# Kernel optimization log

Hardware: AMD Instinct MI355X
Metric: run time of the kernel (lower is better)

## Reference

```python
import jax, jax.numpy as jnp
import numpy as np

B, H, W_, D, K = 64, 28, 28, 512, 32


def setup_inputs() -> dict:
    key = jax.random.key(0)
    k1, k2, k3 = jax.random.split(key, 3)
    x = jax.random.normal(k1, (B, H, W_, D), dtype=jnp.float32)
    # 1x1 conv weight, no bias: [D_in, K] (he_normal-like scale)
    W = jax.random.normal(k2, (D, K), dtype=jnp.float32) * np.sqrt(2.0 / D)
    # cluster offset tensor C (original shape (1,1,1,512,32), squeezed to [D,K])
    C = jax.random.normal(k3, (D, K), dtype=jnp.float32) * np.sqrt(2.0 / D)
    return {"x": x, "W": W, "C": C}


def reference(x, W, C):
    # 1x1 conv == per-pixel matmul: [B,H,W,D] @ [D,K] -> [B,H,W,K]
    s = jnp.einsum('bhwd,dk->bhwk', x, W)
    a = jax.nn.softmax(s, axis=-1)  # soft cluster assignment
    # Original math: v[b,d,k] = sum_{h,w} a[b,h,w,k] * (x[b,h,w,d] + C[d,k])
    # Algebraically identical split avoids the [B,H,W,D,K] 5D intermediate:
    #   sum_hw a*x  (matmul of assignments with features)
    # + (sum_hw a) * C  (cheap correction term)
    v = jnp.einsum('bhwk,bhwd->bdk', a, x) + jnp.sum(a, axis=(1, 2))[:, None, :] * C[None]
    return v.reshape(v.shape[0], -1)  # flatten -> [B, D*K]
```

## Files before the change

### kernel.cpp

```cpp
#include <hip/hip_runtime.h>

#define NB 64
#define HW 784
#define DD 512
#define KK 32
#define BPB 14
#define PPB 56
#define CHUNK 32
#define NCHUNK 2

typedef __attribute__((ext_vector_type(8))) short bf16x8;
typedef __attribute__((ext_vector_type(4))) float f32x4;

#define PART_F   ((size_t)NB * BPB * 8 * 8 * 64 * 4)
#define ASUM_OFF PART_F
#define WS_NEED  ((PART_F + (size_t)NB * BPB * KK) * sizeof(float))

__device__ __forceinline__ unsigned short f2bf(float f) {
    unsigned u = __float_as_uint(f);
    u += 0x7fffu + ((u >> 16) & 1u);
    return (unsigned short)(u >> 16);
}

template <bool USE_WS>
__global__ __launch_bounds__(512) void netvlad_stage1(
    const float* __restrict__ x, const float* __restrict__ Wg,
    const float* __restrict__ Cg, float* __restrict__ out,
    float* __restrict__ ws)
{
    __shared__ __align__(16) unsigned short xs[CHUNK * 520];
    __shared__ float spart[4][CHUNK][33];
    __shared__ __align__(16) unsigned short aTe[KK * 40];
    __shared__ float asumF[KK];

    const int tid = threadIdx.x;
    const int l   = tid & 63, w = tid >> 6;
    const int l15 = l & 15,  lq = l >> 4;
    const int d4  = w & 3;
    const int pgrp= w >> 2;
    const int k   = tid & 31, pg = tid >> 5;
    const int bid = blockIdx.x;
    const int b   = bid / BPB;
    const int pb  = (bid % BPB) * PPB;
    const float* xb = x + (size_t)b * HW * DD;

    bf16x8 Wf[4][2];
#pragma unroll
    for (int ks = 0; ks < 4; ++ks)
#pragma unroll
        for (int nt = 0; nt < 2; ++nt)
#pragma unroll
            for (int j = 0; j < 8; ++j)
                Wf[ks][nt][j] = (short)f2bf(Wg[(d4*128 + ks*32 + lq*8 + j) * KK + nt*16 + l15]);

    f32x4 acc[2][4];
#pragma unroll
    for (int mt = 0; mt < 2; ++mt)
#pragma unroll
        for (int nt = 0; nt < 4; ++nt)
#pragma unroll
            for (int jj = 0; jj < 4; ++jj) acc[mt][nt][jj] = 0.f;
    float asum_part = 0.f;

    auto stageChunk = [&](int c) {
        float4 r[8];
#pragma unroll
        for (int j = 0; j < 8; ++j) {
            const int f = tid + 512*j, row = f >> 7, c4 = f & 127;
            const int p = c*CHUNK + row;
            const int gp = pb + (p < PPB ? p : PPB - 1);
            r[j] = *(const float4*)(xb + (size_t)gp * DD + c4*4);
        }
#pragma unroll
        for (int j = 0; j < 8; ++j) {
            const int f = tid + 512*j, row = f >> 7, c4 = f & 127;
            uint2 pk = make_uint2((unsigned)f2bf(r[j].x) | ((unsigned)f2bf(r[j].y) << 16),
                                  (unsigned)f2bf(r[j].z) | ((unsigned)f2bf(r[j].w) << 16));
            *(uint2*)&xs[row*520 + c4*4] = pk;
        }
    };

    stageChunk(0);
    __syncthreads();

    for (int c = 0; c < NCHUNK; ++c) {
        f32x4 sp[2];
#pragma unroll
        for (int nt = 0; nt < 2; ++nt)
#pragma unroll
            for (int jj = 0; jj < 4; ++jj) sp[nt][jj] = 0.f;
#pragma unroll
        for (int ks = 0; ks < 4; ++ks) {
            const bf16x8 af = *(const bf16x8*)&xs[(pgrp*16 + l15)*520 + d4*128 + ks*32 + lq*8];
#pragma unroll
            for (int nt = 0; nt < 2; ++nt)
                sp[nt] = __builtin_amdgcn_mfma_f32_16x16x32_bf16(
                    af, Wf[ks][nt], sp[nt], 0, 0, 0);
        }
#pragma unroll
        for (int nt = 0; nt < 2; ++nt)
#pragma unroll
            for (int jj = 0; jj < 4; ++jj)
                spart[d4][pgrp*16 + lq*4 + jj][nt*16 + l15] = sp[nt][jj];
        __syncthreads();

        const int valid = (PPB - c*CHUNK < CHUNK) ? (PPB - c*CHUNK) : CHUNK;
#pragma unroll
        for (int i = 0; i < 2; ++i) {
            const int p = pg + 16*i;
            const float s = spart[0][p][k] + spart[1][p][k]
                          + spart[2][p][k] + spart[3][p][k];
            const float e = __expf(s);
            float su = e;
#pragma unroll
            for (int msk = 16; msk >= 1; msk >>= 1)
                su += __shfl_xor(su, msk);
            const float a = (p < valid) ? e * __builtin_amdgcn_rcpf(su) : 0.f;
            asum_part += a;
            aTe[k*40 + p] = f2bf(a);
        }
        __syncthreads();

        bf16x8 afr[2];
#pragma unroll
        for (int mt = 0; mt < 2; ++mt)
            afr[mt] = *(const bf16x8*)&aTe[(mt*16 + l15)*40 + lq*8];
#pragma unroll
        for (int nt = 0; nt < 4; ++nt) {
            const int d = w*64 + nt*16 + l15;
            bf16x8 bfr;
#pragma unroll
            for (int j = 0; j < 8; ++j) {
                const int jj = (j + 2*lq) & 7;
                bfr[jj] = (short)xs[(lq*8 + jj)*520 + d];
            }
#pragma unroll
            for (int mt = 0; mt < 2; ++mt)
                acc[mt][nt] = __builtin_amdgcn_mfma_f32_16x16x32_bf16(
                    afr[mt], bfr, acc[mt][nt], 0, 0, 0);
        }
        __syncthreads();

        if (c + 1 < NCHUNK) {
            stageChunk(c + 1);
            __syncthreads();
        }
    }

    float* ared = (float*)aTe;
    ared[pg*KK + k] = asum_part;
    __syncthreads();
    if (tid < KK) {
        float s = 0.f;
#pragma unroll
        for (int g = 0; g < 16; ++g) s += ared[g*KK + tid];
        if (USE_WS) ws[ASUM_OFF + (size_t)bid * KK + tid] = s;
        else        asumF[tid] = s;
    }

    if (USE_WS) {
        float4* o = (float4*)ws + ((size_t)bid * 8 + w) * (8 * 64);
#pragma unroll
        for (int mt = 0; mt < 2; ++mt)
#pragma unroll
            for (int nt = 0; nt < 4; ++nt)
                o[(mt*4 + nt)*64 + l] = make_float4(acc[mt][nt][0], acc[mt][nt][1],
                                                    acc[mt][nt][2], acc[mt][nt][3]);
    } else {
        __syncthreads();
        float* ob = out + (size_t)b * (DD * KK);
#pragma unroll
        for (int mt = 0; mt < 2; ++mt)
#pragma unroll
            for (int nt = 0; nt < 4; ++nt)
#pragma unroll
                for (int jj = 0; jj < 4; ++jj) {
                    const int kk = mt*16 + lq*4 + jj;
                    const int d  = w*64 + nt*16 + l15;
                    atomicAdd(&ob[d*KK + kk], acc[mt][nt][jj] + asumF[kk] * Cg[d*KK + kk]);
                }
    }
}

__global__ __launch_bounds__(256) void netvlad_stage2(
    const float* __restrict__ ws, const float* __restrict__ Cg,
    float* __restrict__ out)
{
    __shared__ float lds[128 * 33];
    __shared__ float asumT[KK];

    const int t = threadIdx.x;
    const int b = blockIdx.x >> 2;
    const int jsl = blockIdx.x & 3;

    if (t < KK) {
        float s = 0.f;
#pragma unroll
        for (int p = 0; p < BPB; ++p)
            s += ws[ASUM_OFF + (size_t)(b*BPB + p) * KK + t];
        asumT[t] = s;
    }

    const float4* wsp = (const float4*)ws;
    float4 v[4];
#pragma unroll
    for (int i = 0; i < 4; ++i) v[i] = make_float4(0.f, 0.f, 0.f, 0.f);
    for (int p = 0; p < BPB; ++p) {
        const size_t base = (size_t)(b*BPB + p) * 8 * (8 * 64);
#pragma unroll
        for (int i = 0; i < 4; ++i) {
            const int flat = t + 256*i;
            const int g = flat >> 6, lane = flat & 63;
            const int w2 = g >> 3, fr = g & 7;
            const float4 f4 = wsp[base + ((size_t)(2*jsl + w2) * 8 + fr)*64 + lane];
            v[i].x += f4.x; v[i].y += f4.y; v[i].z += f4.z; v[i].w += f4.w;
        }
    }
#pragma unroll
    for (int i = 0; i < 4; ++i) {
        const int flat = t + 256*i;
        const int g = flat >> 6, lane = flat & 63;
        const int w2 = g >> 3, fr = g & 7;
        const int mt = fr >> 2, nt = fr & 3;
        const int q = lane >> 4, r15 = lane & 15;
        const int dl = w2*64 + nt*16 + r15;
        const int kb = mt*16 + q*4;
        lds[dl*33 + kb + 0] = v[i].x;
        lds[dl*33 + kb + 1] = v[i].y;
        lds[dl*33 + kb + 2] = v[i].z;
        lds[dl*33 + kb + 3] = v[i].w;
    }
    __syncthreads();

    float* outw = out + (size_t)b * (DD*KK) + jsl * 128 * KK;
    const float* Cw = Cg + jsl * 128 * KK;
#pragma unroll
    for (int i = 0; i < 4; ++i) {
        const int o4 = t + 256*i;
        const int dl = o4 >> 3, kq = (o4 & 7) * 4;
        const float4 c4 = *(const float4*)&Cw[dl*KK + kq];
        float4 rr;
        rr.x = lds[dl*33 + kq + 0] + asumT[kq + 0] * c4.x;
        rr.y = lds[dl*33 + kq + 1] + asumT[kq + 1] * c4.y;
        rr.z = lds[dl*33 + kq + 2] + asumT[kq + 2] * c4.z;
        rr.w = lds[dl*33 + kq + 3] + asumT[kq + 3] * c4.w;
        ((float4*)outw)[o4] = rr;
    }
}

extern "C" void kernel_launch(void* const* d_in, const int* in_sizes, int n_in,
                              void* d_out, int out_size, void* d_ws, size_t ws_size,
                              hipStream_t stream) {
    const float* x = (const float*)d_in[0];
    const float* W = (const float*)d_in[1];
    const float* C = (const float*)d_in[2];
    float* out = (float*)d_out;

    if (ws_size >= WS_NEED) {
        float* ws = (float*)d_ws;
        netvlad_stage1<true><<<dim3(NB * BPB), dim3(512), 0, stream>>>(x, W, C, out, ws);
        netvlad_stage2<<<dim3(NB * 4), dim3(256), 0, stream>>>(ws, C, out);
    } else {
        hipMemsetAsync(out, 0, (size_t)out_size * sizeof(float), stream);
        netvlad_stage1<false><<<dim3(NB * BPB), dim3(512), 0, stream>>>(x, W, C, out, nullptr);
    }
}
```

Before: 59.43 us.

## Stage x via direct global-to-LDS loads in fp32, convert to bf16 at use

Replaces the register-staged fp32-to-bf16 conversion of input tiles with global_load_lds DMA writes of raw fp32 into shared memory. The bf16 conversion moves to the point where the fragments are read, and the partial logits in shared memory are stored as bf16 instead of fp32. The aim is to cut VGPR pressure and load latency on the staging path. In exchange the x tile in LDS doubles in size, each element is converted once per use, and the logits lose precision before the softmax. There is no explicit wait on the async LDS loads beyond __syncthreads, which may be unsafe.

```diff
diff --git a/kernel.cpp b/kernel.cpp
--- a/kernel.cpp
+++ b/kernel.cpp
@@ -8,6 +8,7 @@
 #define PPB 56
 #define CHUNK 32
 #define NCHUNK 2
+#define XROW 516
 
 typedef __attribute__((ext_vector_type(8))) short bf16x8;
 typedef __attribute__((ext_vector_type(4))) float f32x4;
@@ -20,6 +21,23 @@
     unsigned u = __float_as_uint(f);
     u += 0x7fffu + ((u >> 16) & 1u);
     return (unsigned short)(u >> 16);
+}
+__device__ __forceinline__ float bf2f(unsigned short u) {
+    return __uint_as_float((unsigned)u << 16);
+}
+__device__ __forceinline__ bf16x8 cvt8v(float4 a, float4 b) {
+    bf16x8 r;
+    r[0] = (short)f2bf(a.x); r[1] = (short)f2bf(a.y);
+    r[2] = (short)f2bf(a.z); r[3] = (short)f2bf(a.w);
+    r[4] = (short)f2bf(b.x); r[5] = (short)f2bf(b.y);
+    r[6] = (short)f2bf(b.z); r[7] = (short)f2bf(b.w);
+    return r;
+}
+__device__ __forceinline__ void gload16(const float4* g, float4* l) {
+    __builtin_amdgcn_global_load_lds(
+        (const __attribute__((address_space(1))) unsigned int*)g,
+        (__attribute__((address_space(3))) unsigned int*)l,
+        16, 0, 0);
 }
 
 template <bool USE_WS>
@@ -28,8 +46,8 @@
     const float* __restrict__ Cg, float* __restrict__ out,
     float* __restrict__ ws)
 {
-    __shared__ __align__(16) unsigned short xs[CHUNK * 520];
-    __shared__ float spart[4][CHUNK][33];
+    __shared__ __align__(16) float xs[CHUNK * XROW];
+    __shared__ unsigned short spart[4][CHUNK][34];
     __shared__ __align__(16) unsigned short aTe[KK * 40];
     __shared__ float asumF[KK];
 
@@ -62,25 +80,19 @@
             for (int jj = 0; jj < 4; ++jj) acc[mt][nt][jj] = 0.f;
     float asum_part = 0.f;
 
-    auto stageChunk = [&](int c) {
-        float4 r[8];
+    auto stageIssue = [&](int c) {
 #pragma unroll
         for (int j = 0; j < 8; ++j) {
-            const int f = tid + 512*j, row = f >> 7, c4 = f & 127;
-            const int p = c*CHUNK + row;
+            const int idx = w*8 + j;
+            const int r = idx >> 1, h = idx & 1;
+            const int p = c*CHUNK + r;
             const int gp = pb + (p < PPB ? p : PPB - 1);
-            r[j] = *(const float4*)(xb + (size_t)gp * DD + c4*4);
-        }
-#pragma unroll
-        for (int j = 0; j < 8; ++j) {
-            const int f = tid + 512*j, row = f >> 7, c4 = f & 127;
-            uint2 pk = make_uint2((unsigned)f2bf(r[j].x) | ((unsigned)f2bf(r[j].y) << 16),
-                                  (unsigned)f2bf(r[j].z) | ((unsigned)f2bf(r[j].w) << 16));
-            *(uint2*)&xs[row*520 + c4*4] = pk;
+            gload16((const float4*)(xb + (size_t)gp * DD + h*256) + l,
+                    (float4*)&xs[r*XROW + h*256]);
         }
     };
 
-    stageChunk(0);
+    stageIssue(0);
     __syncthreads();
 
     for (int c = 0; c < NCHUNK; ++c) {
@@ -91,7 +103,8 @@
             for (int jj = 0; jj < 4; ++jj) sp[nt][jj] = 0.f;
 #pragma unroll
         for (int ks = 0; ks < 4; ++ks) {
-            const bf16x8 af = *(const bf16x8*)&xs[(pgrp*16 + l15)*520 + d4*128 + ks*32 + lq*8];
+            const float* pa = &xs[(pgrp*16 + l15)*XROW + d4*128 + ks*32 + lq*8];
+            const bf16x8 af = cvt8v(*(const float4*)pa, *(const float4*)(pa + 4));
 #pragma unroll
             for (int nt = 0; nt < 2; ++nt)
                 sp[nt] = __builtin_amdgcn_mfma_f32_16x16x32_bf16(
@@ -101,15 +114,15 @@
         for (int nt = 0; nt < 2; ++nt)
 #pragma unroll
             for (int jj = 0; jj < 4; ++jj)
-                spart[d4][pgrp*16 + lq*4 + jj][nt*16 + l15] = sp[nt][jj];
+                spart[d4][pgrp*16 + lq*4 + jj][nt*16 + l15] = f2bf(sp[nt][jj]);
         __syncthreads();
 
         const int valid = (PPB - c*CHUNK < CHUNK) ? (PPB - c*CHUNK) : CHUNK;
 #pragma unroll
         for (int i = 0; i < 2; ++i) {
             const int p = pg + 16*i;
-            const float s = spart[0][p][k] + spart[1][p][k]
-                          + spart[2][p][k] + spart[3][p][k];
+            const float s = bf2f(spart[0][p][k]) + bf2f(spart[1][p][k])
+                          + bf2f(spart[2][p][k]) + bf2f(spart[3][p][k]);
             const float e = __expf(s);
             float su = e;
 #pragma unroll
@@ -132,7 +145,7 @@
 #pragma unroll
             for (int j = 0; j < 8; ++j) {
                 const int jj = (j + 2*lq) & 7;
-                bfr[jj] = (short)xs[(lq*8 + jj)*520 + d];
+                bfr[jj] = (short)f2bf(xs[(lq*8 + jj)*XROW + d]);
             }
 #pragma unroll
             for (int mt = 0; mt < 2; ++mt)
@@ -142,7 +155,7 @@
         __syncthreads();
 
         if (c + 1 < NCHUNK) {
-            stageChunk(c + 1);
+            stageIssue(c + 1);
             __syncthreads();
         }
     }
```

Measured after the change: 59.22 us. No clear change (-0.4%).
